# Optimization experiments

Hardware: AMD Instinct MI355X
Metric: run time of the kernel (lower is better)

Reference implementation:

```python
import jax, jax.numpy as jnp
import numpy as np

BLOCK = 64
N_HEADS = 16
HEAD_DIM = 64
HIDDEN = N_HEADS * HEAD_DIM
W_BLOCKS = 3   # sliding window blocks (centered: i-1, i, i+1)
G_BLOCKS = 1   # global blocks (block 0)
LN_EPS = 1e-12
NEG = -1e9


def _build_layout(nblk):
    """Static bigbird-style block layout: per query block, indices of attended key blocks.
    Returns idx [nblk, G+W] int32 and valid [nblk, G+W] bool (dedup'd, range-checked)."""
    nkb = G_BLOCKS + W_BLOCKS
    idx = np.zeros((nblk, nkb), dtype=np.int32)
    valid = np.zeros((nblk, nkb), dtype=bool)
    globals_ = list(range(G_BLOCKS))
    half = W_BLOCKS // 2
    for i in range(nblk):
        cands = globals_ + [i - half + j for j in range(W_BLOCKS)]
        seen = set()
        for c, cand in enumerate(cands):
            ok = (0 <= cand < nblk) and (cand not in seen)
            if ok:
                seen.add(cand)
            idx[i, c] = min(max(cand, 0), nblk - 1)
            valid[i, c] = ok
    return jnp.asarray(idx), jnp.asarray(valid)


def setup_inputs() -> dict:
    key = jax.random.key(0)
    ks = jax.random.split(key, 8)
    b, s = 4, 4096
    sd = 1.0 / np.sqrt(HIDDEN)
    inp = {
        "hidden_states": jax.random.normal(ks[0], (b, s, HIDDEN), dtype=jnp.float32),
        "attention_mask": jnp.zeros((b, s), dtype=jnp.float32),
        "wq": jax.random.normal(ks[1], (HIDDEN, HIDDEN), dtype=jnp.float32) * sd,
        "bq": jnp.zeros((HIDDEN,), dtype=jnp.float32),
        "wk": jax.random.normal(ks[2], (HIDDEN, HIDDEN), dtype=jnp.float32) * sd,
        "bk": jnp.zeros((HIDDEN,), dtype=jnp.float32),
        "wv": jax.random.normal(ks[3], (HIDDEN, HIDDEN), dtype=jnp.float32) * sd,
        "bv": jnp.zeros((HIDDEN,), dtype=jnp.float32),
        "wo": jax.random.normal(ks[4], (HIDDEN, HIDDEN), dtype=jnp.float32) * sd,
        "bo": jnp.zeros((HIDDEN,), dtype=jnp.float32),
        "ln_g": jnp.ones((HIDDEN,), dtype=jnp.float32),
        "ln_b": jnp.zeros((HIDDEN,), dtype=jnp.float32),
    }
    return inp


def _sparse_attention(hidden_states, attention_mask, wq, bq, wk, bk, wv, bv, wo, bo, ln_g, ln_b):
    b, s, h = hidden_states.shape
    nblk = s // BLOCK
    idx, valid = _build_layout(nblk)          # [nblk, nkb]
    nkb = idx.shape[1]

    def proj(w, bias):
        y = hidden_states @ w.T + bias                      # [b, s, H]
        return y.reshape(b, s, N_HEADS, HEAD_DIM).transpose(0, 2, 1, 3)  # [b, h, s, d]

    q = proj(wq, bq)
    k = proj(wk, bk)
    v = proj(wv, bv)

    # blockify: [b, h, nblk, BLOCK, d]
    qb = q.reshape(b, N_HEADS, nblk, BLOCK, HEAD_DIM)
    kb = k.reshape(b, N_HEADS, nblk, BLOCK, HEAD_DIM)
    vb = v.reshape(b, N_HEADS, nblk, BLOCK, HEAD_DIM)

    # gather attended key/value blocks per query block: [b, h, nblk, nkb, BLOCK, d]
    kg = kb[:, :, idx]
    vg = vb[:, :, idx]

    scale = 1.0 / np.sqrt(HEAD_DIM)
    # scores: [b, h, nblk, BLOCK(q), nkb, BLOCK(k)]
    scores = jnp.einsum("bhnqd,bhnmkd->bhnqmk", qb, kg) * scale

    # key padding mask (additive float), gathered to sparse layout
    kp = attention_mask.reshape(b, nblk, BLOCK)[:, idx]      # [b, nblk, nkb, BLOCK]
    scores = scores + kp[:, None, :, None, :, :]
    # invalid (out-of-layout) blocks
    scores = jnp.where(valid[None, None, :, None, :, None], scores, NEG)

    # softmax over all attended keys (nkb * BLOCK)
    flat = scores.reshape(b, N_HEADS, nblk, BLOCK, nkb * BLOCK)
    probs = jax.nn.softmax(flat, axis=-1).reshape(scores.shape)

    ctx = jnp.einsum("bhnqmk,bhnmkd->bhnqd", probs, vg)      # [b, h, nblk, BLOCK, d]
    ctx = ctx.reshape(b, N_HEADS, s, HEAD_DIM).transpose(0, 2, 1, 3).reshape(b, s, h)

    # output projection + residual + LayerNorm (dropout in eval mode = identity)
    y = ctx @ wo.T + bo + hidden_states
    mu = jnp.mean(y, axis=-1, keepdims=True)
    var = jnp.mean((y - mu) ** 2, axis=-1, keepdims=True)
    return (y - mu) * jax.lax.rsqrt(var + LN_EPS) * ln_g + ln_b


def reference(hidden_states, attention_mask, wq, bq, wk, bk, wv, bv, wo, bo, ln_g, ln_b):
    return _sparse_attention(hidden_states, attention_mask, wq, bq, wk, bk, wv, bv, wo, bo, ln_g, ln_b)
```

## Files before the change

kernel.cpp:

```cpp
#include <hip/hip_runtime.h>
#include <cstdint>
#include <cstddef>


using f32x4 = __attribute__((ext_vector_type(4))) float;
using s16x8 = __attribute__((ext_vector_type(8))) short;
using u16x4 = __attribute__((ext_vector_type(4))) unsigned short;

#define NEGV -1000000000.0f

__device__ __forceinline__ unsigned short f2b(float f) {
  unsigned u = __float_as_uint(f);
  u += 0x7FFFu + ((u >> 16) & 1u);
  return (unsigned short)(u >> 16);
}

#define GLDS(g, l)                                                        \
  __builtin_amdgcn_global_load_lds(                                       \
      (__attribute__((address_space(1))) void*)(g),                       \
      (__attribute__((address_space(3))) void*)(l), 16, 0, 0)

__global__ __launch_bounds__(256) void cast_hidden(const float* __restrict__ in,
                                                   unsigned short* __restrict__ out) {
  size_t i = (size_t)blockIdx.x * 256 + threadIdx.x;
  float4 v = ((const float4*)in)[i];
  u16x4 o = {f2b(v.x), f2b(v.y), f2b(v.z), f2b(v.w)};
  ((u16x4*)out)[i] = o;
}

__global__ __launch_bounds__(256) void cast_weights(const float* __restrict__ w0,
                                                    const float* __restrict__ w1,
                                                    const float* __restrict__ w2,
                                                    const float* __restrict__ w3,
                                                    unsigned short* __restrict__ out) {
  const float* src = blockIdx.y == 0 ? w0 : blockIdx.y == 1 ? w1 : blockIdx.y == 2 ? w2 : w3;
  size_t i = (size_t)blockIdx.x * 256 + threadIdx.x;
  float4 v = ((const float4*)src)[i];
  u16x4 o = {f2b(v.x), f2b(v.y), f2b(v.z), f2b(v.w)};
  ((u16x4*)(out + (size_t)blockIdx.y * 1048576))[i] = o;
}

template <int MODE>
__global__ __launch_bounds__(256) void gemm128(const unsigned short* __restrict__ A,
                                               const unsigned short* __restrict__ B,
                                               const float* __restrict__ bias,
                                               const float* __restrict__ resid,
                                               void* __restrict__ outp) {
  __shared__ __align__(16) unsigned short As[4096];
  __shared__ __align__(16) unsigned short Bs[4096];
  const int t = threadIdx.x;
  const int wave = t >> 6, lane = t & 63;
  const int quad = lane >> 4, lr = lane & 15;
  const int wm = (wave >> 1) << 6, wn = (wave & 1) << 6;
  const int bm = blockIdx.x << 7, bn = blockIdx.y << 7;

  f32x4 acc[4][4] = {};

  const int srow = t >> 2;
  const int sq = (t & 3) ^ ((srow >> 1) & 3);
  const char* Ag = (const char*)A + (((size_t)(bm + srow)) << 11) + (sq << 4);
  const char* Bg = (const char*)B + (((size_t)(bn + srow)) << 11) + (sq << 4);
  char* AsW = (char*)As + (t << 4);
  char* BsW = (char*)Bs + (t << 4);

  for (int kt = 0; kt < 2048; kt += 64) {
    __syncthreads();
    GLDS(Ag + kt, AsW);
    GLDS(Ag + kt + (64ll << 11), AsW + 4096);
    GLDS(Bg + kt, BsW);
    GLDS(Bg + kt + (64ll << 11), BsW + 4096);
    __syncthreads();
    s16x8 af[4], bf[4];
#pragma unroll
    for (int i = 0; i < 4; ++i) {
      const int ra = wm + i * 16 + lr;
      af[i] = *(const s16x8*)((const char*)As + ra * 64 + ((quad ^ ((ra >> 1) & 3)) << 4));
      const int rb = wn + i * 16 + lr;
      bf[i] = *(const s16x8*)((const char*)Bs + rb * 64 + ((quad ^ ((rb >> 1) & 3)) << 4));
    }
#pragma unroll
    for (int i = 0; i < 4; ++i)
#pragma unroll
      for (int j = 0; j < 4; ++j)
        acc[i][j] = __builtin_amdgcn_mfma_f32_16x16x32_bf16(af[i], bf[j], acc[i][j], 0, 0, 0);
  }

  float bv[4];
#pragma unroll
  for (int j = 0; j < 4; ++j) bv[j] = bias[bn + wn + j * 16 + lr];

  if (MODE == 0) {
    unsigned short* o = (unsigned short*)outp;
    int hh[4], dd[4];
#pragma unroll
    for (int j = 0; j < 4; ++j) {
      int n = bn + wn + j * 16 + lr;
      hh[j] = n >> 6;
      dd[j] = n & 63;
    }
#pragma unroll
    for (int i = 0; i < 4; ++i) {
#pragma unroll
      for (int r = 0; r < 4; ++r) {
        int m = bm + wm + i * 16 + quad * 4 + r;
        int bb = m >> 12, sl = m & 4095;
        size_t base = ((size_t)bb * 16) * 262144 + (size_t)sl * 64;
#pragma unroll
        for (int j = 0; j < 4; ++j)
          o[base + (size_t)hh[j] * 262144 + dd[j]] = f2b(acc[i][j][r] + bv[j]);
      }
    }
  } else if (MODE == 2) {
    unsigned short* o = (unsigned short*)outp;
    int hh[4], dd[4];
#pragma unroll
    for (int j = 0; j < 4; ++j) {
      int n = bn + wn + j * 16 + lr;
      hh[j] = n >> 6;
      dd[j] = n & 63;
    }
#pragma unroll
    for (int i = 0; i < 4; ++i) {
#pragma unroll
      for (int r = 0; r < 4; ++r) {
        int m = bm + wm + i * 16 + quad * 4 + r;
        int bb = m >> 12, blk = (m >> 6) & 63, mi = m & 63;
        int sg = (mi & 15) * 4 + (mi >> 4);
#pragma unroll
        for (int j = 0; j < 4; ++j)
          o[(((size_t)bb * 16 + hh[j]) * 64 + dd[j]) * 4096 + blk * 64 + sg] =
              f2b(acc[i][j][r] + bv[j]);
      }
    }
  } else {
    float* o = (float*)outp;
#pragma unroll
    for (int i = 0; i < 4; ++i) {
#pragma unroll
      for (int r = 0; r < 4; ++r) {
        size_t m = bm + wm + i * 16 + quad * 4 + r;
        const float* rr = resid + m * 1024 + bn + wn;
        float* orow = o + m * 1024 + bn + wn;
#pragma unroll
        for (int j = 0; j < 4; ++j)
          orow[j * 16 + lr] = acc[i][j][r] + bv[j] + rr[j * 16 + lr];
      }
    }
  }
}

__global__ __launch_bounds__(256) void attn(const unsigned short* __restrict__ Q,
                                            const unsigned short* __restrict__ K,
                                            const unsigned short* __restrict__ vT,
                                            const float* __restrict__ amask,
                                            unsigned short* __restrict__ ctx) {
  __shared__ __align__(16) char smem[69632];
  char* Qs = smem;
  char* Ks = smem + 9216;
  char* Pb = smem;
  char* Vt = smem + 33792;
  float* wmaxL = (float*)(smem + 67584);
  float* wsumL = (float*)(smem + 68608);

  const int qi = blockIdx.x, h = blockIdx.y, b = blockIdx.z;
  const int t = threadIdx.x;
  const int wave = t >> 6, lane = t & 63;
  const int quad = lane >> 4, lr = lane & 15;

  int kb[4], kv[4];
  kb[0] = 0; kv[0] = 1;
#pragma unroll
  for (int c = 1; c < 4; ++c) {
    int cand = qi - 2 + c;
    kv[c] = (cand >= 1 && cand < 64);
    kb[c] = cand < 0 ? 0 : (cand > 63 ? 63 : cand);
  }

  const size_t bh = ((size_t)b * 16 + h) * 262144;
  const unsigned short* Qg = Q + bh + (size_t)qi * 4096;

  {
    int row = t >> 3, ch = t & 7;
    *(s16x8*)(Qs + row * 144 + ch * 16) = *(const s16x8*)((const char*)Qg + row * 128 + ch * 16);
    *(s16x8*)(Qs + (row + 32) * 144 + ch * 16) =
        *(const s16x8*)((const char*)Qg + (row + 32) * 128 + ch * 16);
#pragma unroll
    for (int c = 0; c < 4; ++c) {
      const unsigned short* Kg = K + bh + (size_t)kb[c] * 4096;
      char* Kc = Ks + c * 9216;
      *(s16x8*)(Kc + row * 144 + ch * 16) = *(const s16x8*)((const char*)Kg + row * 128 + ch * 16);
      *(s16x8*)(Kc + (row + 32) * 144 + ch * 16) =
          *(const s16x8*)((const char*)Kg + (row + 32) * 128 + ch * 16);
    }
  }
  float mj[4];
#pragma unroll
  for (int j = 0; j < 4; ++j) {
    float mv = amask[(size_t)b * 4096 + kb[wave] * 64 + j * 16 + lr];
    mj[j] = kv[wave] ? mv : mv + NEGV;
  }
  __syncthreads();

  f32x4 s[4][4] = {};
  const char* Kc = Ks + wave * 9216;
#pragma unroll
  for (int ks = 0; ks < 2; ++ks) {
    s16x8 af[4], bf[4];
#pragma unroll
    for (int i = 0; i < 4; ++i) {
      af[i] = *(const s16x8*)(Qs + (i * 16 + lr) * 144 + ks * 64 + quad * 16);
      bf[i] = *(const s16x8*)(Kc + (i * 16 + lr) * 144 + ks * 64 + quad * 16);
    }
#pragma unroll
    for (int i = 0; i < 4; ++i)
#pragma unroll
      for (int j = 0; j < 4; ++j)
        s[i][j] = __builtin_amdgcn_mfma_f32_16x16x32_bf16(af[i], bf[j], s[i][j], 0, 0, 0);
  }
#pragma unroll
  for (int j = 0; j < 4; ++j)
#pragma unroll
    for (int i = 0; i < 4; ++i)
#pragma unroll
      for (int r = 0; r < 4; ++r) s[i][j][r] = s[i][j][r] * 0.125f + mj[j];
#pragma unroll
  for (int i = 0; i < 4; ++i)
#pragma unroll
    for (int r = 0; r < 4; ++r) {
      float m0 = fmaxf(fmaxf(s[i][0][r], s[i][1][r]), fmaxf(s[i][2][r], s[i][3][r]));
      m0 = fmaxf(m0, __shfl_xor(m0, 1, 64));
      m0 = fmaxf(m0, __shfl_xor(m0, 2, 64));
      m0 = fmaxf(m0, __shfl_xor(m0, 4, 64));
      m0 = fmaxf(m0, __shfl_xor(m0, 8, 64));
      if (lr == 0) wmaxL[(i * 16 + quad * 4 + r) * 4 + wave] = m0;
    }
  __syncthreads();

  {
    int d = t & 63;
    const unsigned short* src = vT + (((size_t)b * 16 + h) * 64 + d) * 4096 + kb[wave] * 64;
    char* dst = Vt + d * 528 + wave * 128;
#pragma unroll
    for (int ch = 0; ch < 8; ++ch)
      *(s16x8*)(dst + ch * 16) = *(const s16x8*)((const char*)src + ch * 16);
  }

#pragma unroll
  for (int i = 0; i < 4; ++i)
#pragma unroll
    for (int r = 0; r < 4; ++r) {
      int row = i * 16 + quad * 4 + r;
      f32x4 wmv = *(const f32x4*)(wmaxL + row * 4);
      float g = fmaxf(fmaxf(wmv[0], wmv[1]), fmaxf(wmv[2], wmv[3]));
      float e0 = __expf(s[i][0][r] - g);
      float e1 = __expf(s[i][1][r] - g);
      float e2 = __expf(s[i][2][r] - g);
      float e3 = __expf(s[i][3][r] - g);
      float sm = (e0 + e1) + (e2 + e3);
      sm += __shfl_xor(sm, 1, 64);
      sm += __shfl_xor(sm, 2, 64);
      sm += __shfl_xor(sm, 4, 64);
      sm += __shfl_xor(sm, 8, 64);
      if (lr == 0) wsumL[row * 4 + wave] = sm;
      u16x4 pv = {f2b(e0), f2b(e1), f2b(e2), f2b(e3)};
      *(u16x4*)(Pb + row * 528 + wave * 128 + lr * 8) = pv;
    }
  __syncthreads();

  f32x4 acc2[4] = {};
  const char* Prow = Pb + (wave * 16 + lr) * 528;
#pragma unroll
  for (int ks = 0; ks < 8; ++ks) {
    s16x8 a = *(const s16x8*)(Prow + ks * 64 + quad * 16);
#pragma unroll
    for (int j = 0; j < 4; ++j) {
      s16x8 bb2 = *(const s16x8*)(Vt + (j * 16 + lr) * 528 + ks * 64 + quad * 16);
      acc2[j] = __builtin_amdgcn_mfma_f32_16x16x32_bf16(a, bb2, acc2[j], 0, 0, 0);
    }
  }
  float inv[4];
#pragma unroll
  for (int r = 0; r < 4; ++r) {
    int row = wave * 16 + quad * 4 + r;
    f32x4 wsv = *(const f32x4*)(wsumL + row * 4);
    inv[r] = 1.0f / (wsv[0] + wsv[1] + wsv[2] + wsv[3]);
  }
#pragma unroll
  for (int r = 0; r < 4; ++r) {
    size_t srow = (size_t)qi * 64 + wave * 16 + quad * 4 + r;
    size_t base = ((size_t)b * 4096 + srow) * 1024 + h * 64;
#pragma unroll
    for (int j = 0; j < 4; ++j) ctx[base + j * 16 + lr] = f2b(acc2[j][r] * inv[r]);
  }
}

__global__ __launch_bounds__(256) void lnorm(float* __restrict__ y,
                                             const float* __restrict__ g,
                                             const float* __restrict__ bta) {
  __shared__ float red[8];
  float4* p = (float4*)(y + (size_t)blockIdx.x * 1024);
  float4 v = p[threadIdx.x];
  float s1 = v.x + v.y + v.z + v.w;
  float s2 = v.x * v.x + v.y * v.y + v.z * v.z + v.w * v.w;
#pragma unroll
  for (int m = 1; m <= 32; m <<= 1) {
    s1 += __shfl_xor(s1, m, 64);
    s2 += __shfl_xor(s2, m, 64);
  }
  int wv = threadIdx.x >> 6;
  if ((threadIdx.x & 63) == 0) {
    red[wv] = s1;
    red[4 + wv] = s2;
  }
  __syncthreads();
  float t1 = red[0] + red[1] + red[2] + red[3];
  float t2 = red[4] + red[5] + red[6] + red[7];
  float mu = t1 * (1.0f / 1024.0f);
  float var = t2 * (1.0f / 1024.0f) - mu * mu;
  float rs = rsqrtf(var + 1e-12f);
  float4 gg = ((const float4*)g)[threadIdx.x];
  float4 bb = ((const float4*)bta)[threadIdx.x];
  float4 o;
  o.x = (v.x - mu) * rs * gg.x + bb.x;
  o.y = (v.y - mu) * rs * gg.y + bb.y;
  o.z = (v.z - mu) * rs * gg.z + bb.z;
  o.w = (v.w - mu) * rs * gg.w + bb.w;
  p[threadIdx.x] = o;
}

extern "C" void kernel_launch(void* const* d_in, const int* in_sizes, int n_in,
                              void* d_out, int out_size, void* d_ws, size_t ws_size,
                              hipStream_t stream) {
  (void)in_sizes; (void)n_in; (void)out_size; (void)ws_size;
  const float* hs = (const float*)d_in[0];
  const float* amask = (const float*)d_in[1];
  const float* wq = (const float*)d_in[2];
  const float* bq = (const float*)d_in[3];
  const float* wk = (const float*)d_in[4];
  const float* bk = (const float*)d_in[5];
  const float* wv = (const float*)d_in[6];
  const float* bv = (const float*)d_in[7];
  const float* wo = (const float*)d_in[8];
  const float* bo = (const float*)d_in[9];
  const float* lg = (const float*)d_in[10];
  const float* lb = (const float*)d_in[11];

  char* ws = (char*)d_ws;
  unsigned short* hbf = (unsigned short*)(ws);
  unsigned short* wqb = (unsigned short*)(ws + 33554432);
  unsigned short* qb  = (unsigned short*)(ws + 41943040);
  unsigned short* kbb = (unsigned short*)(ws + 75497472);
  unsigned short* vtb = (unsigned short*)(ws + 109051904);
  unsigned short* cxb = (unsigned short*)(ws + 142606336);
  unsigned short* wkb = wqb + 1048576;
  unsigned short* wvb = wkb + 1048576;
  unsigned short* wob = wvb + 1048576;
  float* out = (float*)d_out;

  cast_hidden<<<16384, 256, 0, stream>>>(hs, hbf);
  cast_weights<<<dim3(1024, 4), 256, 0, stream>>>(wq, wk, wv, wo, wqb);

  dim3 gg(128, 8);
  gemm128<0><<<gg, 256, 0, stream>>>(hbf, wqb, bq, nullptr, qb);
  gemm128<0><<<gg, 256, 0, stream>>>(hbf, wkb, bk, nullptr, kbb);
  gemm128<2><<<gg, 256, 0, stream>>>(hbf, wvb, bv, nullptr, vtb);

  attn<<<dim3(64, 16, 4), 256, 0, stream>>>(qb, kbb, vtb, amask, cxb);

  gemm128<1><<<gg, 256, 0, stream>>>(cxb, wob, bo, hs, (void*)out);
  lnorm<<<16384, 256, 0, stream>>>(out, lg, lb);
}
```

Measured before the change: 462.7 us.

## Fuse QKV projections into one launch and slim attention shared memory

```diff
diff --git a/kernel.cpp b/kernel.cpp
--- a/kernel.cpp
+++ b/kernel.cpp
@@ -40,22 +40,28 @@
   ((u16x4*)(out + (size_t)blockIdx.y * 1048576))[i] = o;
 }
 
-template <int MODE>
-__global__ __launch_bounds__(256) void gemm128(const unsigned short* __restrict__ A,
-                                               const unsigned short* __restrict__ B,
-                                               const float* __restrict__ bias,
-                                               const float* __restrict__ resid,
-                                               void* __restrict__ outp) {
+__global__ __launch_bounds__(256) void gemm_qkv(const unsigned short* __restrict__ A,
+                                                const unsigned short* __restrict__ Bcat,
+                                                const float* __restrict__ bq,
+                                                const float* __restrict__ bk,
+                                                const float* __restrict__ bv,
+                                                unsigned short* __restrict__ qout,
+                                                unsigned short* __restrict__ kout,
+                                                unsigned short* __restrict__ vtout) {
   __shared__ __align__(16) unsigned short As[4096];
   __shared__ __align__(16) unsigned short Bs[4096];
   const int t = threadIdx.x;
   const int wave = t >> 6, lane = t & 63;
   const int quad = lane >> 4, lr = lane & 15;
   const int wm = (wave >> 1) << 6, wn = (wave & 1) << 6;
-  const int bm = blockIdx.x << 7, bn = blockIdx.y << 7;
+  const int bm = blockIdx.x << 7;
+  const int proj = blockIdx.y >> 3;
+  const int bn = (blockIdx.y & 7) << 7;
+  const unsigned short* B = Bcat + (size_t)proj * 1048576;
+  const float* bias = proj == 0 ? bq : proj == 1 ? bk : bv;
+  unsigned short* o = proj == 0 ? qout : proj == 1 ? kout : vtout;
 
   f32x4 acc[4][4] = {};
-
   const int srow = t >> 2;
   const int sq = (t & 3) ^ ((srow >> 1) & 3);
   const char* Ag = (const char*)A + (((size_t)(bm + srow)) << 11) + (sq << 4);
@@ -85,19 +91,16 @@
         acc[i][j] = __builtin_amdgcn_mfma_f32_16x16x32_bf16(af[i], bf[j], acc[i][j], 0, 0, 0);
   }
 
-  float bv[4];
-#pragma unroll
-  for (int j = 0; j < 4; ++j) bv[j] = bias[bn + wn + j * 16 + lr];
-
-  if (MODE == 0) {
-    unsigned short* o = (unsigned short*)outp;
-    int hh[4], dd[4];
-#pragma unroll
-    for (int j = 0; j < 4; ++j) {
-      int n = bn + wn + j * 16 + lr;
-      hh[j] = n >> 6;
-      dd[j] = n & 63;
-    }
+  float bvv[4];
+  int hh[4], dd[4];
+#pragma unroll
+  for (int j = 0; j < 4; ++j) {
+    int n = bn + wn + j * 16 + lr;
+    bvv[j] = bias[n];
+    hh[j] = n >> 6;
+    dd[j] = n & 63;
+  }
+  if (proj < 2) {
 #pragma unroll
     for (int i = 0; i < 4; ++i) {
 #pragma unroll
@@ -107,18 +110,10 @@
         size_t base = ((size_t)bb * 16) * 262144 + (size_t)sl * 64;
 #pragma unroll
         for (int j = 0; j < 4; ++j)
-          o[base + (size_t)hh[j] * 262144 + dd[j]] = f2b(acc[i][j][r] + bv[j]);
+          o[base + (size_t)hh[j] * 262144 + dd[j]] = f2b(acc[i][j][r] + bvv[j]);
       }
     }
-  } else if (MODE == 2) {
-    unsigned short* o = (unsigned short*)outp;
-    int hh[4], dd[4];
-#pragma unroll
-    for (int j = 0; j < 4; ++j) {
-      int n = bn + wn + j * 16 + lr;
-      hh[j] = n >> 6;
-      dd[j] = n & 63;
-    }
+  } else {
 #pragma unroll
     for (int i = 0; i < 4; ++i) {
 #pragma unroll
@@ -129,38 +124,84 @@
 #pragma unroll
         for (int j = 0; j < 4; ++j)
           o[(((size_t)bb * 16 + hh[j]) * 64 + dd[j]) * 4096 + blk * 64 + sg] =
-              f2b(acc[i][j][r] + bv[j]);
+              f2b(acc[i][j][r] + bvv[j]);
       }
     }
-  } else {
-    float* o = (float*)outp;
+  }
+}
+
+__global__ __launch_bounds__(256) void gemm_out(const unsigned short* __restrict__ A,
+                                                const unsigned short* __restrict__ B,
+                                                const float* __restrict__ bias,
+                                                const float* __restrict__ resid,
+                                                float* __restrict__ o) {
+  __shared__ __align__(16) unsigned short As[4096];
+  __shared__ __align__(16) unsigned short Bs[4096];
+  const int t = threadIdx.x;
+  const int wave = t >> 6, lane = t & 63;
+  const int quad = lane >> 4, lr = lane & 15;
+  const int wm = (wave >> 1) << 6, wn = (wave & 1) << 6;
+  const int bm = blockIdx.x << 7, bn = blockIdx.y << 7;
+
+  f32x4 acc[4][4] = {};
+  const int srow = t >> 2;
+  const int sq = (t & 3) ^ ((srow >> 1) & 3);
+  const char* Ag = (const char*)A + (((size_t)(bm + srow)) << 11) + (sq << 4);
+  const char* Bg = (const char*)B + (((size_t)(bn + srow)) << 11) + (sq << 4);
+  char* AsW = (char*)As + (t << 4);
+  char* BsW = (char*)Bs + (t << 4);
+
+  for (int kt = 0; kt < 2048; kt += 64) {
+    __syncthreads();
+    GLDS(Ag + kt, AsW);
+    GLDS(Ag + kt + (64ll << 11), AsW + 4096);
+    GLDS(Bg + kt, BsW);
+    GLDS(Bg + kt + (64ll << 11), BsW + 4096);
+    __syncthreads();
+    s16x8 af[4], bf[4];
 #pragma unroll
     for (int i = 0; i < 4; ++i) {
-#pragma unroll
-      for (int r = 0; r < 4; ++r) {
-        size_t m = bm + wm + i * 16 + quad * 4 + r;
-        const float* rr = resid + m * 1024 + bn + wn;
-        float* orow = o + m * 1024 + bn + wn;
-#pragma unroll
-        for (int j = 0; j < 4; ++j)
-          orow[j * 16 + lr] = acc[i][j][r] + bv[j] + rr[j * 16 + lr];
-      }
-    }
-  }
-}
-
-__global__ __launch_bounds__(256) void attn(const unsigned short* __restrict__ Q,
-                                            const unsigned short* __restrict__ K,
-                                            const unsigned short* __restrict__ vT,
-                                            const float* __restrict__ amask,
-                                            unsigned short* __restrict__ ctx) {
-  __shared__ __align__(16) char smem[69632];
+      const int ra = wm + i * 16 + lr;
+      af[i] = *(const s16x8*)((const char*)As + ra * 64 + ((quad ^ ((ra >> 1) & 3)) << 4));
+      const int rb = wn + i * 16 + lr;
+      bf[i] = *(const s16x8*)((const char*)Bs + rb * 64 + ((quad ^ ((rb >> 1) & 3)) << 4));
+    }
+#pragma unroll
+    for (int i = 0; i < 4; ++i)
+#pragma unroll
+      for (int j = 0; j < 4; ++j)
+        acc[i][j] = __builtin_amdgcn_mfma_f32_16x16x32_bf16(af[i], bf[j], acc[i][j], 0, 0, 0);
+  }
+
+  float bv[4];
+#pragma unroll
+  for (int j = 0; j < 4; ++j) bv[j] = bias[bn + wn + j * 16 + lr];
+#pragma unroll
+  for (int i = 0; i < 4; ++i) {
+#pragma unroll
+    for (int r = 0; r < 4; ++r) {
+      size_t m = bm + wm + i * 16 + quad * 4 + r;
+      const float* rr = resid + m * 1024 + bn + wn;
+      float* orow = o + m * 1024 + bn + wn;
+#pragma unroll
+      for (int j = 0; j < 4; ++j)
+        orow[j * 16 + lr] = acc[i][j][r] + bv[j] + rr[j * 16 + lr];
+    }
+  }
+}
+
+__global__ __launch_bounds__(256, 3) void attn(const unsigned short* __restrict__ Q,
+                                               const unsigned short* __restrict__ K,
+                                               const unsigned short* __restrict__ vT,
+                                               const float* __restrict__ amask,
+                                               unsigned short* __restrict__ ctx) {
+  __shared__ __align__(16) char smem[51200];
   char* Qs = smem;
-  char* Ks = smem + 9216;
+  char* Ks = smem + 8192;
   char* Pb = smem;
-  char* Vt = smem + 33792;
-  float* wmaxL = (float*)(smem + 67584);
-  float* wsumL = (float*)(smem + 68608);
+  char* Vt = smem + 32768;
+  float* wmaxL = (float*)(smem + 49152);
+  float* wsumL = (float*)(smem + 50176);
 
   const int qi = blockIdx.x, h = blockIdx.y, b = blockIdx.z;
   const int t = threadIdx.x;
@@ -177,20 +218,35 @@
   }
 
   const size_t bh = ((size_t)b * 16 + h) * 262144;
-  const unsigned short* Qg = Q + bh + (size_t)qi * 4096;
-
+
+  s16x8 vreg[2][4];
   {
-    int row = t >> 3, ch = t & 7;
-    *(s16x8*)(Qs + row * 144 + ch * 16) = *(const s16x8*)((const char*)Qg + row * 128 + ch * 16);
-    *(s16x8*)(Qs + (row + 32) * 144 + ch * 16) =
-        *(const s16x8*)((const char*)Qg + (row + 32) * 128 + ch * 16);
-#pragma unroll
-    for (int c = 0; c < 4; ++c) {
-      const unsigned short* Kg = K + bh + (size_t)kb[c] * 4096;
-      char* Kc = Ks + c * 9216;
-      *(s16x8*)(Kc + row * 144 + ch * 16) = *(const s16x8*)((const char*)Kg + row * 128 + ch * 16);
-      *(s16x8*)(Kc + (row + 32) * 144 + ch * 16) =
-          *(const s16x8*)((const char*)Kg + (row + 32) * 128 + ch * 16);
+    const int dl = t >> 3, cs = t & 7;
+    const size_t vrow = ((size_t)b * 16 + h) * 64;
+#pragma unroll
+    for (int p = 0; p < 2; ++p)
+#pragma unroll
+      for (int q = 0; q < 4; ++q) {
+        const char* src = (const char*)(vT + (vrow + p * 32 + dl) * 4096 + kb[q] * 64) +
+                          ((cs ^ (dl & 7)) << 4);
+        vreg[p][q] = *(const s16x8*)src;
+      }
+  }
+
+  {
+    const char* Qg = (const char*)(Q + bh + (size_t)qi * 4096);
+#pragma unroll
+    for (int it = 0; it < 2; ++it) {
+      int C = wave * 128 + it * 64 + lane;
+      int row = C >> 3, cs = C & 7;
+      GLDS(Qg + row * 128 + ((cs ^ (row & 7)) << 4), Qs + (C << 4));
+    }
+    const char* Kg = (const char*)(K + bh + (size_t)kb[wave] * 4096);
+#pragma unroll
+    for (int it = 0; it < 8; ++it) {
+      int C = it * 64 + lane;
+      int row = C >> 3, cs = C & 7;
+      GLDS(Kg + row * 128 + ((cs ^ (row & 7)) << 4), Ks + wave * 8192 + (C << 4));
     }
   }
   float mj[4];
@@ -202,14 +258,14 @@
   __syncthreads();
 
   f32x4 s[4][4] = {};
-  const char* Kc = Ks + wave * 9216;
 #pragma unroll
   for (int ks = 0; ks < 2; ++ks) {
     s16x8 af[4], bf[4];
 #pragma unroll
     for (int i = 0; i < 4; ++i) {
-      af[i] = *(const s16x8*)(Qs + (i * 16 + lr) * 144 + ks * 64 + quad * 16);
-      bf[i] = *(const s16x8*)(Kc + (i * 16 + lr) * 144 + ks * 64 + quad * 16);
+      int sw = ((ks * 4 + quad) ^ (lr & 7)) << 4;
+      af[i] = *(const s16x8*)(Qs + (i * 16 + lr) * 128 + sw);
+      bf[i] = *(const s16x8*)(Ks + wave * 8192 + (i * 16 + lr) * 128 + sw);
     }
 #pragma unroll
     for (int i = 0; i < 4; ++i)
@@ -237,14 +293,11 @@
   __syncthreads();
 
   {
-    int d = t & 63;
-    const unsigned short* src = vT + (((size_t)b * 16 + h) * 64 + d) * 4096 + kb[wave] * 64;
-    char* dst = Vt + d * 528 + wave * 128;
-#pragma unroll
-    for (int ch = 0; ch < 8; ++ch)
-      *(s16x8*)(dst + ch * 16) = *(const s16x8*)((const char*)src + ch * 16);
-  }
-
+    const int dl = t >> 3, cs = t & 7;
+    char* dst = Vt + dl * 512 + (cs << 4);
+#pragma unroll
+    for (int q = 0; q < 4; ++q) *(s16x8*)(dst + q * 128) = vreg[0][q];
+  }
 #pragma unroll
   for (int i = 0; i < 4; ++i)
 #pragma unroll
@@ -263,21 +316,45 @@
       sm += __shfl_xor(sm, 8, 64);
       if (lr == 0) wsumL[row * 4 + wave] = sm;
       u16x4 pv = {f2b(e0), f2b(e1), f2b(e2), f2b(e3)};
-      *(u16x4*)(Pb + row * 528 + wave * 128 + lr * 8) = pv;
+      *(u16x4*)(Pb + row * 512 + ((wave * 8 + ((lr >> 1) ^ (row & 7))) << 4) +
+                ((lr & 1) << 3)) = pv;
     }
   __syncthreads();
 
   f32x4 acc2[4] = {};
-  const char* Prow = Pb + (wave * 16 + lr) * 528;
+  const char* Prow = Pb + (wave * 16 + lr) * 512;
 #pragma unroll
   for (int ks = 0; ks < 8; ++ks) {
-    s16x8 a = *(const s16x8*)(Prow + ks * 64 + quad * 16);
-#pragma unroll
-    for (int j = 0; j < 4; ++j) {
-      s16x8 bb2 = *(const s16x8*)(Vt + (j * 16 + lr) * 528 + ks * 64 + quad * 16);
-      acc2[j] = __builtin_amdgcn_mfma_f32_16x16x32_bf16(a, bb2, acc2[j], 0, 0, 0);
-    }
-  }
+    int cc = ks * 4 + quad;
+    int sw = ((cc & 24) | ((cc & 7) ^ (lr & 7))) << 4;
+    s16x8 a = *(const s16x8*)(Prow + sw);
+#pragma unroll
+    for (int jj = 0; jj < 2; ++jj) {
+      s16x8 bb2 = *(const s16x8*)(Vt + (jj * 16 + lr) * 512 + sw);
+      acc2[jj] = __builtin_amdgcn_mfma_f32_16x16x32_bf16(a, bb2, acc2[jj], 0, 0, 0);
+    }
+  }
+  __syncthreads();
+  {
+    const int dl = t >> 3, cs = t & 7;
+    char* dst = Vt + dl * 512 + (cs << 4);
+#pragma unroll
+    for (int q = 0; q < 4; ++q) *(s16x8*)(dst + q * 128) = vreg[1][q];
+  }
+  __syncthreads();
+
+#pragma unroll
+  for (int ks = 0; ks < 8; ++ks) {
+    int cc = ks * 4 + quad;
+    int sw = ((cc & 24) | ((cc & 7) ^ (lr & 7))) << 4;
+    s16x8 a = *(const s16x8*)(Prow + sw);
+#pragma unroll
+    for (int jj = 0; jj < 2; ++jj) {
+      s16x8 bb2 = *(const s16x8*)(Vt + (jj * 16 + lr) * 512 + sw);
+      acc2[2 + jj] = __builtin_amdgcn_mfma_f32_16x16x32_bf16(a, bb2, acc2[2 + jj], 0, 0, 0);
+    }
+  }
+
   float inv[4];
 #pragma unroll
   for (int r = 0; r < 4; ++r) {
@@ -352,21 +429,16 @@
   unsigned short* kbb = (unsigned short*)(ws + 75497472);
   unsigned short* vtb = (unsigned short*)(ws + 109051904);
   unsigned short* cxb = (unsigned short*)(ws + 142606336);
-  unsigned short* wkb = wqb + 1048576;
-  unsigned short* wvb = wkb + 1048576;
-  unsigned short* wob = wvb + 1048576;
+  unsigned short* wob = wqb + 3145728;
   float* out = (float*)d_out;
 
   cast_hidden<<<16384, 256, 0, stream>>>(hs, hbf);
   cast_weights<<<dim3(1024, 4), 256, 0, stream>>>(wq, wk, wv, wo, wqb);
 
-  dim3 gg(128, 8);
-  gemm128<0><<<gg, 256, 0, stream>>>(hbf, wqb, bq, nullptr, qb);
-  gemm128<0><<<gg, 256, 0, stream>>>(hbf, wkb, bk, nullptr, kbb);
-  gemm128<2><<<gg, 256, 0, stream>>>(hbf, wvb, bv, nullptr, vtb);
+  gemm_qkv<<<dim3(128, 24), 256, 0, stream>>>(hbf, wqb, bq, bk, bv, qb, kbb, vtb);
 
   attn<<<dim3(64, 16, 4), 256, 0, stream>>>(qb, kbb, vtb, amask, cxb);
 
-  gemm128<1><<<gg, 256, 0, stream>>>(cxb, wob, bo, hs, (void*)out);
+  gemm_out<<<dim3(128, 8), 256, 0, stream>>>(cxb, wob, bo, hs, out);
   lnorm<<<16384, 256, 0, stream>>>(out, lg, lb);
 }
```

Result: faster. 434.8 us (-6.0%).
